# Optimization experiments

Measured on AMD Instinct MI355X. Metric: run time of the kernel, lower is better.

Reference implementation:

```python
import jax, jax.numpy as jnp
import numpy as np

K = 3          # kernel_size
STRIDE = 1
ITERS = 3      # num_iterations


def squash(t, axis=-1):
    sn = jnp.sum(t * t, axis=axis, keepdims=True)
    return (sn / (1.0 + sn)) * t / jnp.sqrt(sn)


def setup_inputs() -> dict:
    key = jax.random.key(0)
    k1, k2 = jax.random.split(key)
    B, Nin, H, Cin = 8, 32, 14, 8
    C, Cout = 32, 16
    R = Nin * K * K  # 288 route nodes
    x = jax.random.normal(k1, (B, Nin, H, H, Cin), dtype=jnp.float32)
    route_weights = jax.random.normal(k2, (C, R, Cin, Cout), dtype=jnp.float32)
    return {"x": x, "route_weights": route_weights}


def reference(x, route_weights):
    B, Nin, H, _, Cin = x.shape
    C, R, _, Cout = route_weights.shape
    w = (H - K) // STRIDE + 1

    # Extract all w*w spatial windows at once (instead of the python loop).
    rows = STRIDE * jnp.arange(w)[:, None] + jnp.arange(K)  # [w, K]
    win = x[:, :, rows]            # [B, Nin, w, K, W, Cin]
    win = win[:, :, :, :, rows]    # [B, Nin, w, K, w, K, Cin]
    # route-node order matches .view: (Nin, k, k) flattened
    win = win.transpose(0, 2, 4, 1, 3, 5, 6).reshape(B, w, w, R, Cin)

    priors = jnp.einsum('bpqri,crio->cbpqro', win, route_weights)

    # Dynamic routing (fixed small iteration count -> python loop is fine).
    logits = jnp.zeros_like(priors)
    out = None
    for i in range(ITERS):
        probs = jax.nn.softmax(logits, axis=4)  # softmax over route nodes (dim=2 in torch 5D layout)
        out = squash(jnp.sum(probs * priors, axis=4, keepdims=True))  # [C,B,w,w,1,Cout]
        if i != ITERS - 1:
            logits = logits + jnp.sum(priors * out, axis=-1, keepdims=True)

    out = out[:, :, :, :, 0, :]          # [C, B, w, w, Cout]
    return out.transpose(1, 0, 2, 3, 4)  # [B, C, w, w, Cout]
```

## Files before the change

### kernel.cpp

```cpp
#include <hip/hip_runtime.h>
#include <math.h>

namespace {
constexpr int NIN   = 32;
constexpr int H_    = 14;
constexpr int CIN   = 8;
constexpr int C_    = 32;
constexpr int COUT  = 16;
constexpr int R_    = 288;
constexpr int W_    = 12;
constexpr int NITER = 3;
constexpr int CH    = 32;
constexpr int NCH   = 9;
constexpr size_t XSUB = (size_t)NIN * H_ * H_ * CIN;
}

typedef unsigned int u32;
typedef const __attribute__((address_space(1))) u32* as1_u32p;
typedef __attribute__((address_space(3))) u32* as3_u32p;

__device__ __forceinline__ void async_copy16(const void* g, void* l) {
    __builtin_amdgcn_global_load_lds((as1_u32p)g, (as3_u32p)l, 16, 0, 0);
}
__device__ __forceinline__ float dot4(const float4 a, const float4 b) {
    return fmaf(a.x, b.x, fmaf(a.y, b.y, fmaf(a.z, b.z, a.w * b.w)));
}
__device__ __forceinline__ float dpp_add_xor1(float v) {
    int t = __builtin_amdgcn_update_dpp(0, __float_as_int(v), 0xB1, 0xF, 0xF, true);
    return v + __int_as_float(t);
}
__device__ __forceinline__ float dpp_add_xor2(float v) {
    int t = __builtin_amdgcn_update_dpp(0, __float_as_int(v), 0x4E, 0xF, 0xF, true);
    return v + __int_as_float(t);
}
__device__ __forceinline__ float dpp_add_shr4(float v) {
    int t = __builtin_amdgcn_update_dpp(0, __float_as_int(v), 0x114, 0xF, 0xF, true);
    return v + __int_as_float(t);
}
__device__ __forceinline__ float dpp_add_shr8(float v) {
    int t = __builtin_amdgcn_update_dpp(0, __float_as_int(v), 0x118, 0xF, 0xF, true);
    return v + __int_as_float(t);
}
template <int CTRL>
__device__ __forceinline__ float dpp_bc(float v) {
    return __int_as_float(
        __builtin_amdgcn_update_dpp(0, __float_as_int(v), CTRL, 0xF, 0xF, true));
}

__global__ __launch_bounds__(256)
void caps_routeC(const float* __restrict__ x,
                 const float* __restrict__ rw,
                 float* __restrict__ out)
{
    const int tid = threadIdx.x;
    const int p  = blockIdx.x / W_;
    const int q  = blockIdx.x % W_;
    const int b0 = blockIdx.y * 4;
    const int c  = blockIdx.z;

    __shared__ float4 wbuf[2][1024];
    __shared__ float  sRed[4][2][16];
    __shared__ float  redE[4][2];
    __shared__ float  vS[4][16];

    const int og   = tid & 3;
    const int rl   = tid >> 2;
    const int cr   = rl & 31;
    const int sh   = rl >> 5;
    const int lane = tid & 63;
    const int wv   = tid >> 6;
    const int sA   = sh * 2;

    const float* xq = x + (size_t)(b0 + sA + (og >> 1)) * XSUB + (og & 1) * 4;
    const float4* rwcF4 = (const float4*)(rw + (size_t)c * R_ * CIN * COUT);

    float4 xv;
    auto xld = [&](int k) {
        const int r  = k * CH + cr;
        const int n  = r / 9, rem = r - n * 9;
        const int kh = rem / 3, kw = rem - kh * 3;
        xv = *(const float4*)(xq + ((n * H_ + (p + kh)) * H_ + (q + kw)) * CIN);
    };

    auto stage = [&](int k, int buf) {
        const float4* gchunk = rwcF4 + (size_t)k * (CH * 32);
        #pragma unroll
        for (int t = 0; t < 4; ++t) {
            const int s   = t * 256 + tid;
            const int ii  = s >> 7;
            const int wcr = (s >> 2) & 31;
            async_copy16(gchunk + (wcr * 32 + ii * 4 + (s & 3)),
                         (char*)&wbuf[buf][0] + (t * 256 + (tid & 192)) * 16);
        }
    };

    float4 acc[NCH][2];

    xld(0);
    stage(0, 0);
    #pragma unroll
    for (int k = 0; k < NCH; ++k) {
        __syncthreads();
        if (k + 1 < NCH) stage(k + 1, (k + 1) & 1);
        const float4* wb = &wbuf[k & 1][0];
        const float4 cur = xv;
        float fA[8], fB[8];
        fA[0] = dpp_bc<0x00>(cur.x); fA[1] = dpp_bc<0x00>(cur.y);
        fA[2] = dpp_bc<0x00>(cur.z); fA[3] = dpp_bc<0x00>(cur.w);
        fA[4] = dpp_bc<0x55>(cur.x); fA[5] = dpp_bc<0x55>(cur.y);
        fA[6] = dpp_bc<0x55>(cur.z); fA[7] = dpp_bc<0x55>(cur.w);
        fB[0] = dpp_bc<0xAA>(cur.x); fB[1] = dpp_bc<0xAA>(cur.y);
        fB[2] = dpp_bc<0xAA>(cur.z); fB[3] = dpp_bc<0xAA>(cur.w);
        fB[4] = dpp_bc<0xFF>(cur.x); fB[5] = dpp_bc<0xFF>(cur.y);
        fB[6] = dpp_bc<0xFF>(cur.z); fB[7] = dpp_bc<0xFF>(cur.w);
        if (k + 1 < NCH) xld(k + 1);
        float4 a0 = make_float4(0.f, 0.f, 0.f, 0.f);
        float4 a1 = make_float4(0.f, 0.f, 0.f, 0.f);
        #pragma unroll
        for (int i = 0; i < 8; ++i) {
            const float4 wv4 = wb[i * 128 + cr * 4 + og];
            a0.x = fmaf(fA[i], wv4.x, a0.x);  a1.x = fmaf(fB[i], wv4.x, a1.x);
            a0.y = fmaf(fA[i], wv4.y, a0.y);  a1.y = fmaf(fB[i], wv4.y, a1.y);
            a0.z = fmaf(fA[i], wv4.z, a0.z);  a1.z = fmaf(fB[i], wv4.z, a1.z);
            a0.w = fmaf(fA[i], wv4.w, a0.w);  a1.w = fmaf(fB[i], wv4.w, a1.w);
        }
        acc[k][0] = a0;  acc[k][1] = a1;
    }

    float lgA[NCH], lgB[NCH];
    #pragma unroll
    for (int j = 0; j < NCH; ++j) { lgA[j] = 0.f; lgB[j] = 0.f; }

    for (int it = 0; it < NITER; ++it) {
        float4 s0 = make_float4(0.f, 0.f, 0.f, 0.f);
        float4 s1 = make_float4(0.f, 0.f, 0.f, 0.f);
        float se0 = 0.f, se1 = 0.f;

        if (it == 0) {
            #pragma unroll
            for (int j = 0; j < NCH; ++j) {
                s0.x += acc[j][0].x;  s1.x += acc[j][1].x;
                s0.y += acc[j][0].y;  s1.y += acc[j][1].y;
                s0.z += acc[j][0].z;  s1.z += acc[j][1].z;
                s0.w += acc[j][0].w;  s1.w += acc[j][1].w;
            }
        } else {
            const float4 v0 = *(const float4*)&vS[sA][og * 4];
            const float4 v1 = *(const float4*)&vS[sA + 1][og * 4];
            #pragma unroll
            for (int j = 0; j < NCH; ++j) {
                float d0 = dot4(acc[j][0], v0);
                float d1 = dot4(acc[j][1], v1);
                d0 = dpp_add_xor1(d0);  d1 = dpp_add_xor1(d1);
                d0 = dpp_add_xor2(d0);  d1 = dpp_add_xor2(d1);
                lgA[j] += d0;                 lgB[j] += d1;
                const float e0 = __expf(lgA[j]);
                const float e1 = __expf(lgB[j]);
                se0 += e0;                    se1 += e1;
                s0.x = fmaf(e0, acc[j][0].x, s0.x);  s1.x = fmaf(e1, acc[j][1].x, s1.x);
                s0.y = fmaf(e0, acc[j][0].y, s0.y);  s1.y = fmaf(e1, acc[j][1].y, s1.y);
                s0.z = fmaf(e0, acc[j][0].z, s0.z);  s1.z = fmaf(e1, acc[j][1].z, s1.z);
                s0.w = fmaf(e0, acc[j][0].w, s0.w);  s1.w = fmaf(e1, acc[j][1].w, s1.w);
            }
            se0 = dpp_add_shr4(se0);  se1 = dpp_add_shr4(se1);
            se0 = dpp_add_shr8(se0);  se1 = dpp_add_shr8(se1);
            se0 += __shfl_xor(se0, 16, 64);  se1 += __shfl_xor(se1, 16, 64);
            se0 += __shfl_xor(se0, 32, 64);  se1 += __shfl_xor(se1, 32, 64);
            if (lane == 15) { redE[wv][0] = se0; redE[wv][1] = se1; }
        }

        s0.x = dpp_add_shr4(s0.x);  s1.x = dpp_add_shr4(s1.x);
        s0.y = dpp_add_shr4(s0.y);  s1.y = dpp_add_shr4(s1.y);
        s0.z = dpp_add_shr4(s0.z);  s1.z = dpp_add_shr4(s1.z);
        s0.w = dpp_add_shr4(s0.w);  s1.w = dpp_add_shr4(s1.w);
        s0.x = dpp_add_shr8(s0.x);  s1.x = dpp_add_shr8(s1.x);
        s0.y = dpp_add_shr8(s0.y);  s1.y = dpp_add_shr8(s1.y);
        s0.z = dpp_add_shr8(s0.z);  s1.z = dpp_add_shr8(s1.z);
        s0.w = dpp_add_shr8(s0.w);  s1.w = dpp_add_shr8(s1.w);
        #pragma unroll
        for (int off = 16; off <= 32; off <<= 1) {
            s0.x += __shfl_xor(s0.x, off, 64);  s1.x += __shfl_xor(s1.x, off, 64);
            s0.y += __shfl_xor(s0.y, off, 64);  s1.y += __shfl_xor(s1.y, off, 64);
            s0.z += __shfl_xor(s0.z, off, 64);  s1.z += __shfl_xor(s1.z, off, 64);
            s0.w += __shfl_xor(s0.w, off, 64);  s1.w += __shfl_xor(s1.w, off, 64);
        }
        if (lane >= 12 && lane < 16) {
            *(float4*)&sRed[wv][0][(lane & 3) * 4] = s0;
            *(float4*)&sRed[wv][1][(lane & 3) * 4] = s1;
        }
        __syncthreads();

        if (tid < 64) {
            const int sub = tid >> 4;
            const int o   = tid & 15;
            const int g   = sub >> 1;
            const int l   = sub & 1;
            const float inv = (it == 0)
                ? (1.0f / (float)R_)
                : 1.0f / (redE[g * 2][l] + redE[g * 2 + 1][l]);
            float s = (sRed[g * 2][l][o] + sRed[g * 2 + 1][l][o]) * inv;
            float sn = s * s;
            sn = dpp_add_xor1(sn);
            sn = dpp_add_xor2(sn);
            sn += __shfl_xor(sn, 4, 64);
            sn += __shfl_xor(sn, 8, 64);
            const float v = s * (sqrtf(sn) / (1.0f + sn));
            if (it == NITER - 1) {
                out[((((size_t)(b0 + sub) * C_ + c) * W_ + p) * W_ + q) * COUT + o] = v;
            } else {
                vS[sub][o] = v;
            }
        }
        if (it == NITER - 1) break;
        __syncthreads();
    }
}

extern "C" void kernel_launch(void* const* d_in, const int* in_sizes, int n_in,
                              void* d_out, int out_size, void* d_ws, size_t ws_size,
                              hipStream_t stream) {
    const float* x  = (const float*)d_in[0];
    const float* rw = (const float*)d_in[1];
    float* out = (float*)d_out;
    dim3 grid(W_ * W_, 2, C_);
    caps_routeC<<<grid, 256, 0, stream>>>(x, rw, out);
}
```

Measured before the change: 186.2 us.

## Compute squash redundantly per thread and deepen x prefetch to remove barriers

```diff
diff --git a/kernel.cpp b/kernel.cpp
--- a/kernel.cpp
+++ b/kernel.cpp
@@ -59,9 +59,8 @@
     const int c  = blockIdx.z;
 
     __shared__ float4 wbuf[2][1024];
-    __shared__ float  sRed[4][2][16];
-    __shared__ float  redE[4][2];
-    __shared__ float  vS[4][16];
+    __shared__ float  sRed[2][4][2][16];
+    __shared__ float  redE[2][4][2];
 
     const int og   = tid & 3;
     const int rl   = tid >> 2;
@@ -74,12 +73,12 @@
     const float* xq = x + (size_t)(b0 + sA + (og >> 1)) * XSUB + (og & 1) * 4;
     const float4* rwcF4 = (const float4*)(rw + (size_t)c * R_ * CIN * COUT);
 
-    float4 xv;
-    auto xld = [&](int k) {
+    float4 xvb[2];
+    auto xld = [&](int k, int slot) {
         const int r  = k * CH + cr;
         const int n  = r / 9, rem = r - n * 9;
         const int kh = rem / 3, kw = rem - kh * 3;
-        xv = *(const float4*)(xq + ((n * H_ + (p + kh)) * H_ + (q + kw)) * CIN);
+        xvb[slot] = *(const float4*)(xq + ((n * H_ + (p + kh)) * H_ + (q + kw)) * CIN);
     };
 
     auto stage = [&](int k, int buf) {
@@ -96,14 +95,14 @@
 
     float4 acc[NCH][2];
 
-    xld(0);
+    xld(0, 0);
+    xld(1, 1);
     stage(0, 0);
     #pragma unroll
     for (int k = 0; k < NCH; ++k) {
         __syncthreads();
         if (k + 1 < NCH) stage(k + 1, (k + 1) & 1);
-        const float4* wb = &wbuf[k & 1][0];
-        const float4 cur = xv;
+        const float4 cur = xvb[k & 1];
         float fA[8], fB[8];
         fA[0] = dpp_bc<0x00>(cur.x); fA[1] = dpp_bc<0x00>(cur.y);
         fA[2] = dpp_bc<0x00>(cur.z); fA[3] = dpp_bc<0x00>(cur.w);
@@ -113,7 +112,8 @@
         fB[2] = dpp_bc<0xAA>(cur.z); fB[3] = dpp_bc<0xAA>(cur.w);
         fB[4] = dpp_bc<0xFF>(cur.x); fB[5] = dpp_bc<0xFF>(cur.y);
         fB[6] = dpp_bc<0xFF>(cur.z); fB[7] = dpp_bc<0xFF>(cur.w);
-        if (k + 1 < NCH) xld(k + 1);
+        if (k + 2 < NCH) xld(k + 2, k & 1);
+        const float4* wb = &wbuf[k & 1][0];
         float4 a0 = make_float4(0.f, 0.f, 0.f, 0.f);
         float4 a1 = make_float4(0.f, 0.f, 0.f, 0.f);
         #pragma unroll
@@ -131,7 +131,10 @@
     #pragma unroll
     for (int j = 0; j < NCH; ++j) { lgA[j] = 0.f; lgB[j] = 0.f; }
 
+    float4 v0, v1;
+
     for (int it = 0; it < NITER; ++it) {
+        const int par = it & 1;
         float4 s0 = make_float4(0.f, 0.f, 0.f, 0.f);
         float4 s1 = make_float4(0.f, 0.f, 0.f, 0.f);
         float se0 = 0.f, se1 = 0.f;
@@ -145,8 +148,6 @@
                 s0.w += acc[j][0].w;  s1.w += acc[j][1].w;
             }
         } else {
-            const float4 v0 = *(const float4*)&vS[sA][og * 4];
-            const float4 v1 = *(const float4*)&vS[sA + 1][og * 4];
             #pragma unroll
             for (int j = 0; j < NCH; ++j) {
                 float d0 = dot4(acc[j][0], v0);
@@ -166,7 +167,7 @@
             se0 = dpp_add_shr8(se0);  se1 = dpp_add_shr8(se1);
             se0 += __shfl_xor(se0, 16, 64);  se1 += __shfl_xor(se1, 16, 64);
             se0 += __shfl_xor(se0, 32, 64);  se1 += __shfl_xor(se1, 32, 64);
-            if (lane == 15) { redE[wv][0] = se0; redE[wv][1] = se1; }
+            if (lane == 15) { redE[par][wv][0] = se0; redE[par][wv][1] = se1; }
         }
 
         s0.x = dpp_add_shr4(s0.x);  s1.x = dpp_add_shr4(s1.x);
@@ -185,34 +186,42 @@
             s0.w += __shfl_xor(s0.w, off, 64);  s1.w += __shfl_xor(s1.w, off, 64);
         }
         if (lane >= 12 && lane < 16) {
-            *(float4*)&sRed[wv][0][(lane & 3) * 4] = s0;
-            *(float4*)&sRed[wv][1][(lane & 3) * 4] = s1;
+            *(float4*)&sRed[par][wv][0][(lane & 3) * 4] = s0;
+            *(float4*)&sRed[par][wv][1][(lane & 3) * 4] = s1;
         }
         __syncthreads();
 
-        if (tid < 64) {
-            const int sub = tid >> 4;
-            const int o   = tid & 15;
-            const int g   = sub >> 1;
-            const int l   = sub & 1;
-            const float inv = (it == 0)
-                ? (1.0f / (float)R_)
-                : 1.0f / (redE[g * 2][l] + redE[g * 2 + 1][l]);
-            float s = (sRed[g * 2][l][o] + sRed[g * 2 + 1][l][o]) * inv;
-            float sn = s * s;
-            sn = dpp_add_xor1(sn);
-            sn = dpp_add_xor2(sn);
-            sn += __shfl_xor(sn, 4, 64);
-            sn += __shfl_xor(sn, 8, 64);
-            const float v = s * (sqrtf(sn) / (1.0f + sn));
-            if (it == NITER - 1) {
-                out[((((size_t)(b0 + sub) * C_ + c) * W_ + p) * W_ + q) * COUT + o] = v;
-            } else {
-                vS[sub][o] = v;
-            }
-        }
-        if (it == NITER - 1) break;
-        __syncthreads();
+        const float4 pa0 = *(const float4*)&sRed[par][sh * 2    ][0][og * 4];
+        const float4 pb0 = *(const float4*)&sRed[par][sh * 2 + 1][0][og * 4];
+        const float4 pa1 = *(const float4*)&sRed[par][sh * 2    ][1][og * 4];
+        const float4 pb1 = *(const float4*)&sRed[par][sh * 2 + 1][1][og * 4];
+        float inv0, inv1;
+        if (it == 0) {
+            inv0 = inv1 = 1.0f / (float)R_;
+        } else {
+            inv0 = 1.0f / (redE[par][sh * 2][0] + redE[par][sh * 2 + 1][0]);
+            inv1 = 1.0f / (redE[par][sh * 2][1] + redE[par][sh * 2 + 1][1]);
+        }
+        float4 sc0, sc1;
+        sc0.x = (pa0.x + pb0.x) * inv0;  sc1.x = (pa1.x + pb1.x) * inv1;
+        sc0.y = (pa0.y + pb0.y) * inv0;  sc1.y = (pa1.y + pb1.y) * inv1;
+        sc0.z = (pa0.z + pb0.z) * inv0;  sc1.z = (pa1.z + pb1.z) * inv1;
+        sc0.w = (pa0.w + pb0.w) * inv0;  sc1.w = (pa1.w + pb1.w) * inv1;
+        float sn0 = dot4(sc0, sc0);
+        float sn1 = dot4(sc1, sc1);
+        sn0 = dpp_add_xor1(sn0);  sn1 = dpp_add_xor1(sn1);
+        sn0 = dpp_add_xor2(sn0);  sn1 = dpp_add_xor2(sn1);
+        const float f0 = sqrtf(sn0) / (1.0f + sn0);
+        const float f1 = sqrtf(sn1) / (1.0f + sn1);
+        v0.x = sc0.x * f0;  v1.x = sc1.x * f1;
+        v0.y = sc0.y * f0;  v1.y = sc1.y * f1;
+        v0.z = sc0.z * f0;  v1.z = sc1.z * f1;
+        v0.w = sc0.w * f0;  v1.w = sc1.w * f1;
+    }
+
+    if (cr == 0) {
+        *(float4*)&out[((((size_t)(b0 + sA)     * C_ + c) * W_ + p) * W_ + q) * COUT + og * 4] = v0;
+        *(float4*)&out[((((size_t)(b0 + sA + 1) * C_ + c) * W_ + p) * W_ + q) * COUT + og * 4] = v1;
     }
 }
 
```

After: 197.9 us. +6.3%, slower.
